# Kernel optimization log

Measured on AMD Instinct MI355X. Metric: run time of the kernel, lower is better.

## Reference

```python
import jax, jax.numpy as jnp
import numpy as np
from jax import lax

D_MODEL = 384
D_INNER = 768          # expand * d_model
D_HALF = D_INNER // 2  # 384
D_STATE = 16
D_CONV = 4
DT_RANK = 24           # ceil(384/16)
BATCH = 8
SEQLEN = 4097
EXTRAS = 1
LMAIN = SEQLEN - EXTRAS


def setup_inputs() -> dict:
    key = jax.random.key(0)
    ks = jax.random.split(key, 12)
    hidden_states = jax.random.normal(ks[0], (BATCH, SEQLEN, D_MODEL), jnp.float32)
    in_proj_w = jax.random.normal(ks[1], (D_INNER, D_MODEL), jnp.float32) * 0.02
    conv_x_w = jax.random.normal(ks[2], (D_HALF, 1, D_CONV), jnp.float32) * 0.2
    conv_z_w = jax.random.normal(ks[3], (D_HALF, 1, D_CONV), jnp.float32) * 0.2
    x_proj_w = jax.random.normal(ks[4], (DT_RANK + 2 * D_STATE, D_HALF), jnp.float32) * 0.02
    dt_std = DT_RANK ** -0.5
    dt_proj_w = jax.random.uniform(ks[5], (D_HALF, DT_RANK), jnp.float32, -dt_std, dt_std)
    # bias = inverse softplus of dt sampled log-uniform in [1e-3, 1e-1]
    dt = jnp.exp(jax.random.uniform(ks[6], (D_HALF,), jnp.float32)
                 * (jnp.log(0.1) - jnp.log(0.001)) + jnp.log(0.001))
    dt = jnp.clip(dt, 1e-4, None)
    dt_proj_b = dt + jnp.log(-jnp.expm1(-dt))
    A_log = jnp.log(jnp.broadcast_to(jnp.arange(1, D_STATE + 1, dtype=jnp.float32),
                                     (D_HALF, D_STATE)))
    D_param = jnp.ones((D_HALF,), jnp.float32)
    out_proj_w = jax.random.normal(ks[7], (D_MODEL, D_HALF), jnp.float32) * 0.02
    perm = jax.random.permutation(ks[8], LMAIN).astype(jnp.int64)
    perm_rev = jnp.argsort(perm).astype(jnp.int64)
    return {
        "hidden_states": hidden_states,
        "in_proj_w": in_proj_w,
        "conv_x_w": conv_x_w,
        "conv_z_w": conv_z_w,
        "x_proj_w": x_proj_w,
        "dt_proj_w": dt_proj_w,
        "dt_proj_b": dt_proj_b,
        "A_log": A_log,
        "D_param": D_param,
        "out_proj_w": out_proj_w,
        "perm": perm,
        "perm_rev": perm_rev,
    }


def _depthwise_conv_same(x, w):
    # x: (B, C, L), w: (C, 1, K); torch padding='same' for k=4 -> pad (left=1, right=2)
    total = D_CONV - 1
    left = total // 2
    return lax.conv_general_dilated(
        x, w, window_strides=(1,), padding=[(left, total - left)],
        dimension_numbers=("NCH", "OIH", "NCH"), feature_group_count=D_HALF)


def _selective_scan(x, dt, A, Bm, Cm, D_param, delta_bias):
    # x, dt: (B, d, L); A: (d, n); Bm, Cm: (B, n, L)
    dt = jax.nn.softplus(dt + delta_bias[None, :, None])
    xT = jnp.moveaxis(x, 2, 0)    # (L, B, d)
    dtT = jnp.moveaxis(dt, 2, 0)  # (L, B, d)
    BT = jnp.moveaxis(Bm, 2, 0)   # (L, B, n)
    CT = jnp.moveaxis(Cm, 2, 0)   # (L, B, n)

    def step(h, inp):
        x_t, dt_t, B_t, C_t = inp
        dA = jnp.exp(dt_t[..., None] * A)                      # (B, d, n)
        h = h * dA + (dt_t * x_t)[..., None] * B_t[:, None, :]  # (B, d, n)
        y = jnp.einsum("bdn,bn->bd", h, C_t)
        return h, y

    h0 = jnp.zeros((x.shape[0], x.shape[1], A.shape[1]), x.dtype)
    _, ys = lax.scan(step, h0, (xT, dtT, BT, CT))
    y = jnp.moveaxis(ys, 0, 2)  # (B, d, L)
    return y + D_param[None, :, None] * x


def reference(hidden_states, in_proj_w, conv_x_w, conv_z_w, x_proj_w,
              dt_proj_w, dt_proj_b, A_log, D_param, out_proj_w, perm, perm_rev):
    # in_proj (no bias): (B,L,D) -> (B, d_inner, L)
    xz = jnp.einsum("bld,ed->bel", hidden_states, in_proj_w)
    # hilbert/zigzag reorder on the main (non-extra) tokens
    xz = jnp.concatenate([xz[:, :, :EXTRAS], xz[:, :, EXTRAS:][:, :, perm]], axis=2)

    x, z = jnp.split(xz, 2, axis=1)  # (B, d_half, L) each
    A = -jnp.exp(A_log)
    x = jax.nn.silu(_depthwise_conv_same(x, conv_x_w))
    z = jax.nn.silu(_depthwise_conv_same(z, conv_z_w))

    x_dbl = jnp.einsum("bdl,ed->bel", x, x_proj_w)  # (B, dt_rank+2n, L)
    dt_low, Bm, Cm = jnp.split(x_dbl, [DT_RANK, DT_RANK + D_STATE], axis=1)
    dt = jnp.einsum("brl,dr->bdl", dt_low, dt_proj_w)

    y = _selective_scan(x, dt, A, Bm, Cm, D_param, dt_proj_b)
    y = (y * z).transpose(0, 2, 1)  # (B, L, d_half)
    out = jnp.einsum("bld,ed->ble", y, out_proj_w)  # (B, L, D)
    # undo the permutation on the output
    out = jnp.concatenate([out[:, :EXTRAS], out[:, EXTRAS:][:, perm_rev]], axis=1)
    return out
```

## Files before the change

### kernel.cpp

```cpp
#include <hip/hip_runtime.h>
#include <hip/hip_bf16.h>

#define DEVI __device__ __forceinline__

constexpr int B_   = 8;
constexpr int L_   = 4097;
constexpr int MTOT = B_ * L_;
constexpr int DH   = 384;
constexpr int NS   = 16;
constexpr int CH   = 48;
constexpr int NCH  = (L_ + CH - 1) / CH;

typedef __bf16 bf16x8 __attribute__((ext_vector_type(8)));
typedef float  f32x4  __attribute__((ext_vector_type(4)));

DEVI float bl(unsigned v) { return __uint_as_float(v << 16); }
DEVI float bh(unsigned v) { return __uint_as_float(v & 0xffff0000u); }
DEVI float bf(const __hip_bfloat16 x) { return __bfloat162float(x); }
DEVI unsigned short f2bu(float x) {
  __hip_bfloat16 b = __float2bfloat16(x);
  return *(unsigned short*)&b;
}
DEVI float u16f(const uint4& u, int j) {
  const unsigned w = (&u.x)[j >> 1];
  return (j & 1) ? bh(w) : bl(w);
}
DEVI float softplus_f(float x) {
  return (x > 20.f) ? x : __logf(1.f + __expf(x));
}

DEVI void gld16(const __hip_bfloat16* g, __hip_bfloat16* l) {
  __builtin_amdgcn_global_load_lds(
      (const __attribute__((address_space(1))) void*)g,
      (__attribute__((address_space(3))) void*)l, 16, 0, 0);
}

__global__ void flag_k(const void* hs, int* flagp) {
  if (threadIdx.x == 0 && blockIdx.x == 0) {
    const unsigned short* u = (const unsigned short*)hs;
    int ok = 1;
    for (int i = 0; i < 8; ++i) {
      const unsigned short v = u[2 * i];
      const int e = (v >> 7) & 0xFF;
      if (!(v == 0 || (e >= 100 && e <= 140))) ok = 0;
    }
    flagp[0] = ok;
    flagp[1] = 1;
  }
}

__global__ void a2prep_k(const void* __restrict__ alog, float* __restrict__ a2fo,
                         int* flagp) {
  const int d = threadIdx.x;
  const int f = flagp[0];
  float a2[16];
#pragma unroll
  for (int n = 0; n < 16; ++n) {
    const float v = f ? bf(((const __hip_bfloat16*)alog)[d * 16 + n])
                      : ((const float*)alog)[d * 16 + n];
    a2[n] = -1.4426950408889634f * __expf(v);
    a2fo[d * 16 + n] = a2[n];
  }
  int ok = 1;
#pragma unroll
  for (int n = 1; n < 16; ++n) {
    const float ref = (float)(n + 1) * a2[0];
    if (fabsf(a2[n] - ref) > 1e-3f * fabsf(ref)) ok = 0;
  }
  if (!ok) atomicAnd(&flagp[1], 0);
}

__global__ void perm_k(const int* p0, const int* p1, int* d0, int* d1) {
  __shared__ int s_or;
  const int* src = blockIdx.x ? p1 : p0;
  int*       dst = blockIdx.x ? d1 : d0;
  if (threadIdx.x == 0) s_or = 0;
  __syncthreads();
  int loc = 0;
  for (int i = threadIdx.x; i < 2048; i += 1024) loc |= src[2 * i + 1];
  atomicOr(&s_or, loc);
  __syncthreads();
  const bool is64 = (s_or == 0);
  for (int j = threadIdx.x; j < 4096; j += 1024)
    dst[j] = is64 ? (int)((const long long*)src)[j] : src[j];
}

struct NormSet { const void* src[8]; void* dst[8]; int n[8]; };
__global__ void norm_all(NormSet s, const int* flagp) {
  const int idx = blockIdx.x * 256 + threadIdx.x;
  const int f = flagp[0];
#pragma unroll
  for (int t = 0; t < 8; ++t) {
    if (idx < s.n[t]) {
      __hip_bfloat16* d = (__hip_bfloat16*)s.dst[t];
      if (f) d[idx] = ((const __hip_bfloat16*)s.src[t])[idx];
      else   d[idx] = __float2bfloat16(((const float*)s.src[t])[idx]);
    }
  }
}

__global__ void prep_k(const __hip_bfloat16* __restrict__ dtw,
                       const __hip_bfloat16* __restrict__ xw,
                       __hip_bfloat16* __restrict__ wcomb) {
  const int idx = blockIdx.x * 256 + threadIdx.x;
  if (idx >= 512 * 384) return;
  const int n = idx / 384, k = idx - n * 384;
  float v = 0.f;
  if (n < 384) {
#pragma unroll
    for (int r = 0; r < 24; ++r) v += bf(dtw[n * 24 + r]) * bf(xw[r * 384 + k]);
  } else if (n < 416) {
    v = bf(xw[(24 + n - 384) * 384 + k]);
  }
  wcomb[idx] = __float2bfloat16(v);
}

__global__ void cvt_k(const void* __restrict__ hs, __hip_bfloat16* __restrict__ dst,
                      const int* __restrict__ gidx, const int* __restrict__ flagp) {
  const int idx = blockIdx.x * 256 + threadIdx.x;
  if (idx >= MTOT * 48) return;
  const int j = idx % 48;
  const int r = idx / 48;
  const int b = r / L_, t = r - b * L_;
  const int src = b * L_ + (t == 0 ? 0 : 1 + gidx[t - 1]);
  uint4 o;
  if (flagp[0]) {
    o = *(const uint4*)((const __hip_bfloat16*)hs + (size_t)src * 384 + j * 8);
  } else {
    const float* f = (const float*)hs + (size_t)src * 384 + j * 8;
    const float4 f0 = *(const float4*)f;
    const float4 f1 = *(const float4*)(f + 4);
    o.x = f2bu(f0.x) | ((unsigned)f2bu(f0.y) << 16);
    o.y = f2bu(f0.z) | ((unsigned)f2bu(f0.w) << 16);
    o.z = f2bu(f1.x) | ((unsigned)f2bu(f1.y) << 16);
    o.w = f2bu(f1.z) | ((unsigned)f2bu(f1.w) << 16);
  }
  *(uint4*)(dst + (size_t)r * 384 + j * 8) = o;
}

template<int GATHER, int EPI>
__global__ __launch_bounds__(256, 3)
void gemm_k(const __hip_bfloat16* __restrict__ A, const __hip_bfloat16* __restrict__ W,
            void* __restrict__ e0, void* __restrict__ e1,
            const __hip_bfloat16* __restrict__ bias,
            const int* __restrict__ gidx, const int* __restrict__ flagp,
            int M, int N)
{
  __shared__ __align__(16) __hip_bfloat16 lA[128 * 32];
  __shared__ __align__(16) __hip_bfloat16 lB[128 * 32];
  const int tid  = threadIdx.x;
  const int lane = tid & 63;
  const int wv   = tid >> 6;
  const int wm   = wv >> 1, wn = wv & 1;
  const int lrow = lane & 15, quad = lane >> 4;
  const int fbf  = flagp[0];

  const int NT = gridDim.x;
  const int nblocks = NT * (int)gridDim.y;
  const int id = blockIdx.y * NT + blockIdx.x;
  const int q8 = nblocks >> 3, r8 = nblocks & 7;
  const int xcd = id & 7, slot = id >> 3;
  const int nid = (xcd < r8 ? xcd * (q8 + 1)
                            : r8 * (q8 + 1) + (xcd - r8) * q8) + slot;
  const int mt = nid / NT, nt = nid - mt * NT;

  const bool live = !(EPI == 1 && nt * 128 + wn * 64 >= 416);

  const __hip_bfloat16* aSrc[2];
  const __hip_bfloat16* bSrc[2];
  __hip_bfloat16* aDst[2];
  __hip_bfloat16* bDst[2];
#pragma unroll
  for (int p = 0; p < 2; ++p) {
    const int row = p * 64 + (tid >> 2);
    const int kc  = (tid & 3) * 8;
    int r = mt * 128 + row;
    if (r >= M) r = M - 1;
    int src;
    if (GATHER) { const int b = r / L_, t = r - b * L_;
                  src = b * L_ + (t == 0 ? 0 : 1 + gidx[t - 1]); }
    else        { src = r; }
    aSrc[p] = A + (size_t)src * 384 + kc;
    const int c = nt * 128 + row;
    bSrc[p] = W + (size_t)c * 384 + kc;
    aDst[p] = &lA[(p * 256 + tid) * 8];
    bDst[p] = &lB[(p * 256 + tid) * 8];
  }

  f32x4 acc[4][4] = {};

#pragma unroll
  for (int kt = 0; kt < 12; ++kt) {
    __syncthreads();
#pragma unroll
    for (int p = 0; p < 2; ++p) gld16(aSrc[p] + kt * 32, aDst[p]);
#pragma unroll
    for (int p = 0; p < 2; ++p) gld16(bSrc[p] + kt * 32, bDst[p]);
    __syncthreads();
    if (live) {
      bf16x8 af[4], bfr[4];
#pragma unroll
      for (int i = 0; i < 4; ++i)
        af[i] = *reinterpret_cast<const bf16x8*>(&lA[(wm * 64 + i * 16 + lrow) * 32 + quad * 8]);
#pragma unroll
      for (int j = 0; j < 4; ++j)
        bfr[j] = *reinterpret_cast<const bf16x8*>(&lB[(wn * 64 + j * 16 + lrow) * 32 + quad * 8]);
#pragma unroll
      for (int i = 0; i < 4; ++i)
#pragma unroll
        for (int j = 0; j < 4; ++j)
          acc[i][j] = __builtin_amdgcn_mfma_f32_16x16x32_bf16(af[i], bfr[j], acc[i][j], 0, 0, 0);
    }
  }

#pragma unroll
  for (int i = 0; i < 4; ++i) {
    const int row0 = mt * 128 + wm * 64 + i * 16 + quad * 4;
#pragma unroll
    for (int j = 0; j < 4; ++j) {
      const int col = nt * 128 + wn * 64 + j * 16 + lrow;
      if (col >= N) continue;
#pragma unroll
      for (int rg = 0; rg < 4; ++rg) {
        const int r = row0 + rg;
        if (r >= M) continue;
        const float v = acc[i][j][rg];
        if (EPI == 0) {
          if (col < 384) ((__hip_bfloat16*)e0)[(size_t)r * 384 + col] = __float2bfloat16(v);
          else           ((__hip_bfloat16*)e1)[(size_t)r * 384 + (col - 384)] = __float2bfloat16(v);
        } else if (EPI == 1) {
          if (col < 384) {
            const float sp = softplus_f(v + bf(bias[col]));
            ((__hip_bfloat16*)e0)[(size_t)r * 384 + col] = __float2bfloat16(sp);
          } else if (col < 416) {
            ((float*)e1)[(size_t)r * 32 + (col - 384)] = v;
          }
        } else {
          if (fbf) ((__hip_bfloat16*)e0)[(size_t)r * 384 + col] = __float2bfloat16(v);
          else     ((float*)e0)[(size_t)r * 384 + col] = v;
        }
      }
    }
  }
}

__global__ void convx_k(const __hip_bfloat16* __restrict__ xh,
                        const __hip_bfloat16* __restrict__ cxw,
                        __hip_bfloat16* __restrict__ xc) {
  const int idx = blockIdx.x * 256 + threadIdx.x;
  if (idx >= MTOT * 48) return;
  const int g  = idx % 48;
  const int rg = idx / 48;
  const int t  = rg % L_;
  const int c0 = g * 8;
  uint4 wv[4];
#pragma unroll
  for (int p = 0; p < 4; ++p) wv[p] = *(const uint4*)(cxw + c0 * 4 + p * 8);
  float acc[8] = {};
#pragma unroll
  for (int k = 0; k < 4; ++k) {
    const int tt = t + k - 1;
    if (tt < 0 || tt >= L_) continue;
    const uint4 u = *(const uint4*)(xh + (size_t)(rg + k - 1) * 384 + c0);
#pragma unroll
    for (int j = 0; j < 8; ++j) {
      const int e = j * 4 + k;
      acc[j] += u16f(wv[e >> 3], e & 7) * u16f(u, j);
    }
  }
  uint4 o;
#pragma unroll
  for (int p = 0; p < 4; ++p) {
    const float s0 = acc[2 * p]     / (1.f + __expf(-acc[2 * p]));
    const float s1 = acc[2 * p + 1] / (1.f + __expf(-acc[2 * p + 1]));
    (&o.x)[p] = f2bu(s0) | ((unsigned)f2bu(s1) << 16);
  }
  *(uint4*)(xc + (size_t)rg * 384 + c0) = o;
}

__global__ __launch_bounds__(128)
void scan1_k(const __hip_bfloat16* __restrict__ dt, const float* __restrict__ bc,
             __hip_bfloat16* xcio,
             const float* __restrict__ a2f,
             const __hip_bfloat16* __restrict__ dpar,
             float* __restrict__ pbuf, float* __restrict__ hend,
             const int* __restrict__ flagp)
{
  __shared__ __align__(16) float lBC[CH * 32];
  const int blk = blockIdx.x;
  const int dt3 = blk % 3;
  const int c   = (blk / 3) % NCH;
  const int b   = blk / (3 * NCH);
  const int d   = dt3 * 128 + threadIdx.x;
  const int t0  = c * CH;
  const int r0  = b * L_ + t0;
  const int tmax = (L_ - t0 < CH) ? (L_ - t0) : CH;
  for (int i = threadIdx.x; i < tmax * 32; i += 128) lBC[i] = bc[(size_t)r0 * 32 + i];
  __syncthreads();

  float h[16];
#pragma unroll
  for (int n = 0; n < 16; ++n) h[n] = 0.f;
  float sdt = 0.f;
  const float Dd = bf(dpar[d]);
  const size_t base = ((size_t)(c * 8 + b) * 16) * 384 + d;

  if (flagp[1]) {
    const float a2b = a2f[d * 16];
    for (int tt = 0; tt < tmax; ++tt) {
      const size_t r = (size_t)(r0 + tt);
      const float dtv = bf(dt[r * 384 + d]);
      const float xv  = bf(xcio[r * 384 + d]);
      sdt += dtv;
      const float dtx = dtv * xv;
      float pw[17];
      pw[1] = exp2f(dtv * a2b);
#pragma unroll
      for (int n = 2; n <= 16; ++n) pw[n] = pw[n >> 1] * pw[n - (n >> 1)];
      float4 bq[4], cq[4];
#pragma unroll
      for (int q = 0; q < 4; ++q) {
        bq[q] = *(const float4*)&lBC[tt * 32 + q * 4];
        cq[q] = *(const float4*)&lBC[tt * 32 + 16 + q * 4];
      }
      float y = 0.f;
#pragma unroll
      for (int n = 0; n < 16; ++n) {
        h[n] = h[n] * pw[n + 1] + dtx * (&bq[n >> 2].x)[n & 3];
        y += h[n] * (&cq[n >> 2].x)[n & 3];
      }
      y += Dd * xv;
      xcio[r * 384 + d] = __float2bfloat16(y);
    }
    float Ep[17];
    Ep[1] = exp2f(sdt * a2b);
#pragma unroll
    for (int n = 2; n <= 16; ++n) Ep[n] = Ep[n >> 1] * Ep[n - (n >> 1)];
#pragma unroll
    for (int n = 0; n < 16; ++n) {
      pbuf[base + n * 384] = Ep[n + 1];
      hend[base + n * 384] = h[n];
    }
  } else {
    float a2[16];
#pragma unroll
    for (int n = 0; n < 16; ++n) a2[n] = a2f[d * 16 + n];
    for (int tt = 0; tt < tmax; ++tt) {
      const size_t r = (size_t)(r0 + tt);
      const float dtv = bf(dt[r * 384 + d]);
      const float xv  = bf(xcio[r * 384 + d]);
      sdt += dtv;
      const float dtx = dtv * xv;
      float4 bq[4], cq[4];
#pragma unroll
      for (int q = 0; q < 4; ++q) {
        bq[q] = *(const float4*)&lBC[tt * 32 + q * 4];
        cq[q] = *(const float4*)&lBC[tt * 32 + 16 + q * 4];
      }
      float y = 0.f;
#pragma unroll
      for (int n = 0; n < 16; ++n) {
        h[n] = h[n] * exp2f(dtv * a2[n]) + dtx * (&bq[n >> 2].x)[n & 3];
        y += h[n] * (&cq[n >> 2].x)[n & 3];
      }
      y += Dd * xv;
      xcio[r * 384 + d] = __float2bfloat16(y);
    }
#pragma unroll
    for (int n = 0; n < 16; ++n) {
      pbuf[base + n * 384] = exp2f(sdt * a2[n]);
      hend[base + n * 384] = h[n];
    }
  }
}

__global__ void scan2_k(float* __restrict__ pbuf, const float* __restrict__ hend) {
  const int tid = blockIdx.x * 256 + threadIdx.x;
  const int d = tid % 384;
  const int n = (tid / 384) & 15;
  const int b = tid / 6144;
  float H = 0.f;
  for (int c = 0; c < NCH; ++c) {
    const size_t idx = ((size_t)(c * 8 + b) * 16 + n) * 384 + d;
    const float p = pbuf[idx];
    const float he = hend[idx];
    pbuf[idx] = H;
    H = p * H + he;
  }
}

__global__ __launch_bounds__(128)
void scan3_k(__hip_bfloat16* dtyg, const float* __restrict__ bc,
             const __hip_bfloat16* __restrict__ yl,
             const __hip_bfloat16* __restrict__ zh,
             const __hip_bfloat16* __restrict__ czw,
             const float* __restrict__ a2f,
             const float* __restrict__ hstart,
             const int* __restrict__ flagp)
{
  __shared__ __align__(16) float lC[CH * 16];
  const int blk = blockIdx.x;
  const int dt3 = blk % 3;
  const int c   = (blk / 3) % NCH;
  const int b   = blk / (3 * NCH);
  const int d   = dt3 * 128 + threadIdx.x;
  const int t0  = c * CH;
  const int r0  = b * L_ + t0;
  const int tmax = (L_ - t0 < CH) ? (L_ - t0) : CH;
  for (int i = threadIdx.x; i < tmax * 16; i += 128)
    lC[i] = bc[(size_t)r0 * 32 + (i >> 4) * 32 + 16 + (i & 15)];
  __syncthreads();

  float hs_[16];
  const size_t base = ((size_t)(c * 8 + b) * 16) * 384 + d;
#pragma unroll
  for (int n = 0; n < 16; ++n) hs_[n] = hstart[base + n * 384];
  float cw[4];
#pragma unroll
  for (int k = 0; k < 4; ++k) cw[k] = bf(czw[d * 4 + k]);

  float zm1 = (t0 - 1 >= 0) ? bf(zh[(size_t)(r0 - 1) * 384 + d]) : 0.f;
  float z0  = bf(zh[(size_t)r0 * 384 + d]);
  float zp1 = (t0 + 1 < L_) ? bf(zh[(size_t)(r0 + 1) * 384 + d]) : 0.f;
  float sdt = 0.f;

  if (flagp[1]) {
    const float a2b = a2f[d * 16];
    for (int tt = 0; tt < tmax; ++tt) {
      const int t = t0 + tt;
      const size_t r = (size_t)(r0 + tt);
      const float zp2 = (t + 2 < L_) ? bf(zh[(r + 2) * 384 + d]) : 0.f;
      const float dtv = bf(dtyg[r * 384 + d]);
      sdt += dtv;
      float pw[17];
      pw[1] = exp2f(sdt * a2b);
#pragma unroll
      for (int n = 2; n <= 16; ++n) pw[n] = pw[n >> 1] * pw[n - (n >> 1)];
      float4 cq[4];
#pragma unroll
      for (int q = 0; q < 4; ++q) cq[q] = *(const float4*)&lC[tt * 16 + q * 4];
      float corr = 0.f;
#pragma unroll
      for (int n = 0; n < 16; ++n)
        corr += (&cq[n >> 2].x)[n & 3] * hs_[n] * pw[n + 1];
      const float y = bf(yl[r * 384 + d]) + corr;
      const float zc = cw[0] * zm1 + cw[1] * z0 + cw[2] * zp1 + cw[3] * zp2;
      const float zs = zc / (1.f + __expf(-zc));
      dtyg[r * 384 + d] = __float2bfloat16(y * zs);
      zm1 = z0; z0 = zp1; zp1 = zp2;
    }
  } else {
    float a2[16];
#pragma unroll
    for (int n = 0; n < 16; ++n) a2[n] = a2f[d * 16 + n];
    for (int tt = 0; tt < tmax; ++tt) {
      const int t = t0 + tt;
      const size_t r = (size_t)(r0 + tt);
      const float zp2 = (t + 2 < L_) ? bf(zh[(r + 2) * 384 + d]) : 0.f;
      const float dtv = bf(dtyg[r * 384 + d]);
      sdt += dtv;
      float4 cq[4];
#pragma unroll
      for (int q = 0; q < 4; ++q) cq[q] = *(const float4*)&lC[tt * 16 + q * 4];
      float corr = 0.f;
#pragma unroll
      for (int n = 0; n < 16; ++n)
        corr += (&cq[n >> 2].x)[n & 3] * hs_[n] * exp2f(sdt * a2[n]);
      const float y = bf(yl[r * 384 + d]) + corr;
      const float zc = cw[0] * zm1 + cw[1] * z0 + cw[2] * zp1 + cw[3] * zp2;
      const float zs = zc / (1.f + __expf(-zc));
      dtyg[r * 384 + d] = __float2bfloat16(y * zs);
      zm1 = z0; z0 = zp1; zp1 = zp2;
    }
  }
}

extern "C" void kernel_launch(void* const* d_in, const int* in_sizes, int n_in,
                              void* d_out, int out_size, void* d_ws, size_t ws_size,
                              hipStream_t stream) {
  const void* hs   = d_in[0];
  const void* w_in = d_in[1];
  const void* cxw  = d_in[2];
  const void* czw  = d_in[3];
  const void* xw   = d_in[4];
  const void* dtw  = d_in[5];
  const void* dtb  = d_in[6];
  const void* alog = d_in[7];
  const void* dpar = d_in[8];
  const void* ow   = d_in[9];
  const int* perm  = (const int*)d_in[10];
  const int* permr = (const int*)d_in[11];

  char* ws = (char*)d_ws;
  size_t off = 0;
  auto alloc = [&](size_t nbytes) -> char* {
    char* p = ws + off;
    off += (nbytes + 255) & ~(size_t)255;
    return p;
  };
  int* flag              = (int*)alloc(256);
  int* nperm             = (int*)alloc(4096 * 4);
  int* npermr            = (int*)alloc(4096 * 4);
  float* a2f             = (float*)alloc(6144 * 4);
  __hip_bfloat16* w_inb  = (__hip_bfloat16*)alloc(294912 * 2);
  __hip_bfloat16* cxwb   = (__hip_bfloat16*)alloc(1536 * 2);
  __hip_bfloat16* czwb   = (__hip_bfloat16*)alloc(1536 * 2);
  __hip_bfloat16* xwb    = (__hip_bfloat16*)alloc(21504 * 2);
  __hip_bfloat16* dtwb   = (__hip_bfloat16*)alloc(9216 * 2);
  __hip_bfloat16* dtbb   = (__hip_bfloat16*)alloc(384 * 2);
  __hip_bfloat16* dparb  = (__hip_bfloat16*)alloc(384 * 2);
  __hip_bfloat16* owb    = (__hip_bfloat16*)alloc(147456 * 2);
  __hip_bfloat16* wcombb = (__hip_bfloat16*)alloc((size_t)512 * 384 * 2);
  __hip_bfloat16* hsb    = (__hip_bfloat16*)alloc((size_t)MTOT * 384 * 2);
  __hip_bfloat16* zh     = (__hip_bfloat16*)alloc((size_t)MTOT * 384 * 2);
  __hip_bfloat16* xc     = (__hip_bfloat16*)alloc((size_t)MTOT * 384 * 2);
  __hip_bfloat16* dtyg   = (__hip_bfloat16*)alloc((size_t)MTOT * 384 * 2);
  float*          bcf    = (float*)alloc((size_t)MTOT * 32 * 4);
  __hip_bfloat16* xh   = (__hip_bfloat16*)d_out;
  float*          pbuf = (float*)d_out;
  float*          hend = (float*)((char*)d_out + (size_t)NCH * B_ * NS * DH * 4);

  flag_k<<<1, 64, 0, stream>>>(hs, flag);
  perm_k<<<2, 1024, 0, stream>>>(perm, permr, nperm, npermr);
  a2prep_k<<<1, 384, 0, stream>>>(alog, a2f, flag);
  NormSet ns;
  ns.src[0] = w_in; ns.dst[0] = w_inb; ns.n[0] = 294912;
  ns.src[1] = ow;   ns.dst[1] = owb;   ns.n[1] = 147456;
  ns.src[2] = xw;   ns.dst[2] = xwb;   ns.n[2] = 21504;
  ns.src[3] = dtw;  ns.dst[3] = dtwb;  ns.n[3] = 9216;
  ns.src[4] = cxw;  ns.dst[4] = cxwb;  ns.n[4] = 1536;
  ns.src[5] = czw;  ns.dst[5] = czwb;  ns.n[5] = 1536;
  ns.src[6] = dtb;  ns.dst[6] = dtbb;  ns.n[6] = 384;
  ns.src[7] = dpar; ns.dst[7] = dparb; ns.n[7] = 384;
  norm_all<<<1152, 256, 0, stream>>>(ns, flag);
  prep_k<<<768, 256, 0, stream>>>(dtwb, xwb, wcombb);
  cvt_k<<<(MTOT * 48 + 255) / 256, 256, 0, stream>>>(hs, hsb, nperm, flag);
  gemm_k<0, 0><<<dim3(6, 257), 256, 0, stream>>>(
      hsb, w_inb, xh, zh, nullptr, nullptr, flag, MTOT, 768);
  convx_k<<<(MTOT * 48 + 255) / 256, 256, 0, stream>>>(xh, cxwb, xc);
  gemm_k<0, 1><<<dim3(4, 257), 256, 0, stream>>>(
      xc, wcombb, dtyg, bcf, dtbb, nullptr, flag, MTOT, 512);
  scan1_k<<<B_ * NCH * 3, 128, 0, stream>>>(dtyg, bcf, xc, a2f, dparb, pbuf, hend, flag);
  scan2_k<<<192, 256, 0, stream>>>(pbuf, hend);
  scan3_k<<<B_ * NCH * 3, 128, 0, stream>>>(dtyg, bcf, xc, zh, czwb, a2f, pbuf, flag);
  gemm_k<1, 2><<<dim3(3, 257), 256, 0, stream>>>(
      dtyg, owb, d_out, nullptr, nullptr, npermr, flag, MTOT, 384);
  (void)in_sizes; (void)n_in; (void)out_size; (void)ws_size;
}
```

Before: 384.5 us.

## Deepen GEMM K-tile, stage epilogue through LDS, split scan reductions, shrink chunk

The GEMM now loads a K-slice of 64 per iteration, halving the syncthreads-bounded steps. Its epilogue stages accumulators through shared memory so global stores become coalesced 16-byte writes instead of scattered scalar bf16/float stores, with softplus and bias applied before staging. The scan kernels split each 16-term dot-product reduction into two accumulators to shorten the dependent add chain. The scan chunk length drops from 48 to 33, giving more parallel chunks at the cost of more carry-propagation work and larger intermediate buffers. Shared memory per GEMM block grows to 36 KB, which may limit occupancy under the launch bound of 3 blocks.

```diff
diff --git a/kernel.cpp b/kernel.cpp
--- a/kernel.cpp
+++ b/kernel.cpp
@@ -8,7 +8,7 @@
 constexpr int MTOT = B_ * L_;
 constexpr int DH   = 384;
 constexpr int NS   = 16;
-constexpr int CH   = 48;
+constexpr int CH   = 33;
 constexpr int NCH  = (L_ + CH - 1) / CH;
 
 typedef __bf16 bf16x8 __attribute__((ext_vector_type(8)));
@@ -146,8 +146,9 @@
             const int* __restrict__ gidx, const int* __restrict__ flagp,
             int M, int N)
 {
-  __shared__ __align__(16) __hip_bfloat16 lA[128 * 32];
-  __shared__ __align__(16) __hip_bfloat16 lB[128 * 32];
+  __shared__ __align__(16) char smem[36864];
+  __hip_bfloat16* lA = (__hip_bfloat16*)smem;
+  __hip_bfloat16* lB = lA + 2 * 128 * 32;
   const int tid  = threadIdx.x;
   const int lane = tid & 63;
   const int wv   = tid >> 6;
@@ -166,14 +167,16 @@
 
   const bool live = !(EPI == 1 && nt * 128 + wn * 64 >= 416);
 
-  const __hip_bfloat16* aSrc[2];
-  const __hip_bfloat16* bSrc[2];
-  __hip_bfloat16* aDst[2];
-  __hip_bfloat16* bDst[2];
-#pragma unroll
-  for (int p = 0; p < 2; ++p) {
-    const int row = p * 64 + (tid >> 2);
-    const int kc  = (tid & 3) * 8;
+  const __hip_bfloat16* aSrc[4];
+  const __hip_bfloat16* bSrc[4];
+  __hip_bfloat16* aDst[4];
+  __hip_bfloat16* bDst[4];
+#pragma unroll
+  for (int p = 0; p < 4; ++p) {
+    const int s   = p * 256 + tid;
+    const int kh  = s >> 9;
+    const int row = (s >> 2) & 127;
+    const int kc  = kh * 32 + (s & 3) * 8;
     int r = mt * 128 + row;
     if (r >= M) r = M - 1;
     int src;
@@ -181,63 +184,122 @@
                   src = b * L_ + (t == 0 ? 0 : 1 + gidx[t - 1]); }
     else        { src = r; }
     aSrc[p] = A + (size_t)src * 384 + kc;
-    const int c = nt * 128 + row;
-    bSrc[p] = W + (size_t)c * 384 + kc;
-    aDst[p] = &lA[(p * 256 + tid) * 8];
-    bDst[p] = &lB[(p * 256 + tid) * 8];
+    bSrc[p] = W + (size_t)(nt * 128 + row) * 384 + kc;
+    aDst[p] = &lA[s * 8];
+    bDst[p] = &lB[s * 8];
   }
 
   f32x4 acc[4][4] = {};
 
 #pragma unroll
-  for (int kt = 0; kt < 12; ++kt) {
+  for (int kt = 0; kt < 6; ++kt) {
     __syncthreads();
 #pragma unroll
-    for (int p = 0; p < 2; ++p) gld16(aSrc[p] + kt * 32, aDst[p]);
-#pragma unroll
-    for (int p = 0; p < 2; ++p) gld16(bSrc[p] + kt * 32, bDst[p]);
+    for (int p = 0; p < 4; ++p) gld16(aSrc[p] + kt * 64, aDst[p]);
+#pragma unroll
+    for (int p = 0; p < 4; ++p) gld16(bSrc[p] + kt * 64, bDst[p]);
     __syncthreads();
     if (live) {
-      bf16x8 af[4], bfr[4];
-#pragma unroll
-      for (int i = 0; i < 4; ++i)
-        af[i] = *reinterpret_cast<const bf16x8*>(&lA[(wm * 64 + i * 16 + lrow) * 32 + quad * 8]);
-#pragma unroll
-      for (int j = 0; j < 4; ++j)
-        bfr[j] = *reinterpret_cast<const bf16x8*>(&lB[(wn * 64 + j * 16 + lrow) * 32 + quad * 8]);
-#pragma unroll
-      for (int i = 0; i < 4; ++i)
+#pragma unroll
+      for (int kh = 0; kh < 2; ++kh) {
+        bf16x8 af[4], bfr[4];
+#pragma unroll
+        for (int i = 0; i < 4; ++i)
+          af[i] = *reinterpret_cast<const bf16x8*>(
+              &lA[kh * 4096 + (wm * 64 + i * 16 + lrow) * 32 + quad * 8]);
 #pragma unroll
         for (int j = 0; j < 4; ++j)
-          acc[i][j] = __builtin_amdgcn_mfma_f32_16x16x32_bf16(af[i], bfr[j], acc[i][j], 0, 0, 0);
-    }
-  }
-
-#pragma unroll
-  for (int i = 0; i < 4; ++i) {
-    const int row0 = mt * 128 + wm * 64 + i * 16 + quad * 4;
-#pragma unroll
-    for (int j = 0; j < 4; ++j) {
-      const int col = nt * 128 + wn * 64 + j * 16 + lrow;
-      if (col >= N) continue;
-#pragma unroll
-      for (int rg = 0; rg < 4; ++rg) {
-        const int r = row0 + rg;
-        if (r >= M) continue;
-        const float v = acc[i][j][rg];
-        if (EPI == 0) {
-          if (col < 384) ((__hip_bfloat16*)e0)[(size_t)r * 384 + col] = __float2bfloat16(v);
-          else           ((__hip_bfloat16*)e1)[(size_t)r * 384 + (col - 384)] = __float2bfloat16(v);
-        } else if (EPI == 1) {
-          if (col < 384) {
-            const float sp = softplus_f(v + bf(bias[col]));
-            ((__hip_bfloat16*)e0)[(size_t)r * 384 + col] = __float2bfloat16(sp);
-          } else if (col < 416) {
-            ((float*)e1)[(size_t)r * 32 + (col - 384)] = v;
-          }
-        } else {
-          if (fbf) ((__hip_bfloat16*)e0)[(size_t)r * 384 + col] = __float2bfloat16(v);
-          else     ((float*)e0)[(size_t)r * 384 + col] = v;
+          bfr[j] = *reinterpret_cast<const bf16x8*>(
+              &lB[kh * 4096 + (wn * 64 + j * 16 + lrow) * 32 + quad * 8]);
+#pragma unroll
+        for (int i = 0; i < 4; ++i)
+#pragma unroll
+          for (int j = 0; j < 4; ++j)
+            acc[i][j] = __builtin_amdgcn_mfma_f32_16x16x32_bf16(af[i], bfr[j], acc[i][j], 0, 0, 0);
+      }
+    }
+  }
+
+  const int r0c = mt * 128;
+  if (EPI == 1 && nt == 3) {
+#pragma unroll
+    for (int i = 0; i < 4; ++i) {
+      const int row0 = r0c + wm * 64 + i * 16 + quad * 4;
+#pragma unroll
+      for (int j = 0; j < 4; ++j) {
+        const int col = 384 + wn * 64 + j * 16 + lrow;
+        if (col >= 416) continue;
+#pragma unroll
+        for (int rg = 0; rg < 4; ++rg) {
+          const int r = row0 + rg;
+          if (r >= M) continue;
+          ((float*)e1)[(size_t)r * 32 + (col - 384)] = acc[i][j][rg];
+        }
+      }
+    }
+  } else if (EPI == 2 && !fbf) {
+    float* lT = (float*)smem;
+#pragma unroll
+    for (int h = 0; h < 2; ++h) {
+      __syncthreads();
+      if (wn == h) {
+#pragma unroll
+        for (int i = 0; i < 4; ++i)
+#pragma unroll
+          for (int j = 0; j < 4; ++j)
+#pragma unroll
+            for (int rg = 0; rg < 4; ++rg)
+              lT[(wm * 64 + i * 16 + quad * 4 + rg) * 72 + j * 16 + lrow] = acc[i][j][rg];
+      }
+      __syncthreads();
+#pragma unroll
+      for (int p = 0; p < 8; ++p) {
+        const int ch = p * 256 + tid;
+        const int row = ch >> 4, c4 = (ch & 15) * 4;
+        const int r = r0c + row;
+        if (r < M) {
+          const float4 v = *(const float4*)&lT[row * 72 + c4];
+          *(float4*)((float*)e0 + (size_t)r * 384 + nt * 128 + h * 64 + c4) = v;
+        }
+      }
+    }
+  } else {
+    __hip_bfloat16* lT = (__hip_bfloat16*)smem;
+#pragma unroll
+    for (int h = 0; h < 2; ++h) {
+      __syncthreads();
+      if (wn == h) {
+        float bj[4] = {};
+        if (EPI == 1) {
+#pragma unroll
+          for (int j = 0; j < 4; ++j)
+            bj[j] = bf(bias[nt * 128 + h * 64 + j * 16 + lrow]);
+        }
+#pragma unroll
+        for (int i = 0; i < 4; ++i)
+#pragma unroll
+          for (int j = 0; j < 4; ++j)
+#pragma unroll
+            for (int rg = 0; rg < 4; ++rg) {
+              float v = acc[i][j][rg];
+              if (EPI == 1) v = softplus_f(v + bj[j]);
+              lT[(wm * 64 + i * 16 + quad * 4 + rg) * 72 + j * 16 + lrow] =
+                  __float2bfloat16(v);
+            }
+      }
+      __syncthreads();
+#pragma unroll
+      for (int p = 0; p < 4; ++p) {
+        const int ch = p * 256 + tid;
+        const int row = ch >> 3, c8 = (ch & 7) * 8;
+        const int r = r0c + row;
+        if (r < M) {
+          const uint4 v = *(const uint4*)&lT[row * 72 + c8];
+          const int g = nt * 128 + h * 64 + c8;
+          __hip_bfloat16* dst = (EPI == 0 && g >= 384)
+                ? (__hip_bfloat16*)e1 + (size_t)r * 384 + (g - 384)
+                : (__hip_bfloat16*)e0 + (size_t)r * 384 + g;
+          *(uint4*)dst = v;
         }
       }
     }
@@ -323,13 +385,14 @@
         bq[q] = *(const float4*)&lBC[tt * 32 + q * 4];
         cq[q] = *(const float4*)&lBC[tt * 32 + 16 + q * 4];
       }
-      float y = 0.f;
+      float ya = 0.f, yb = 0.f;
 #pragma unroll
       for (int n = 0; n < 16; ++n) {
         h[n] = h[n] * pw[n + 1] + dtx * (&bq[n >> 2].x)[n & 3];
-        y += h[n] * (&cq[n >> 2].x)[n & 3];
-      }
-      y += Dd * xv;
+        const float t = h[n] * (&cq[n >> 2].x)[n & 3];
+        if (n & 1) yb += t; else ya += t;
+      }
+      const float y = ya + yb + Dd * xv;
       xcio[r * 384 + d] = __float2bfloat16(y);
     }
     float Ep[17];
@@ -357,13 +420,14 @@
         bq[q] = *(const float4*)&lBC[tt * 32 + q * 4];
         cq[q] = *(const float4*)&lBC[tt * 32 + 16 + q * 4];
       }
-      float y = 0.f;
+      float ya = 0.f, yb = 0.f;
 #pragma unroll
       for (int n = 0; n < 16; ++n) {
         h[n] = h[n] * exp2f(dtv * a2[n]) + dtx * (&bq[n >> 2].x)[n & 3];
-        y += h[n] * (&cq[n >> 2].x)[n & 3];
-      }
-      y += Dd * xv;
+        const float t = h[n] * (&cq[n >> 2].x)[n & 3];
+        if (n & 1) yb += t; else ya += t;
+      }
+      const float y = ya + yb + Dd * xv;
       xcio[r * 384 + d] = __float2bfloat16(y);
     }
 #pragma unroll
@@ -439,11 +503,13 @@
       float4 cq[4];
 #pragma unroll
       for (int q = 0; q < 4; ++q) cq[q] = *(const float4*)&lC[tt * 16 + q * 4];
-      float corr = 0.f;
-#pragma unroll
-      for (int n = 0; n < 16; ++n)
-        corr += (&cq[n >> 2].x)[n & 3] * hs_[n] * pw[n + 1];
-      const float y = bf(yl[r * 384 + d]) + corr;
+      float ca = 0.f, cb = 0.f;
+#pragma unroll
+      for (int n = 0; n < 16; ++n) {
+        const float t2 = (&cq[n >> 2].x)[n & 3] * hs_[n] * pw[n + 1];
+        if (n & 1) cb += t2; else ca += t2;
+      }
+      const float y = bf(yl[r * 384 + d]) + ca + cb;
       const float zc = cw[0] * zm1 + cw[1] * z0 + cw[2] * zp1 + cw[3] * zp2;
       const float zs = zc / (1.f + __expf(-zc));
       dtyg[r * 384 + d] = __float2bfloat16(y * zs);
@@ -462,11 +528,13 @@
       float4 cq[4];
 #pragma unroll
       for (int q = 0; q < 4; ++q) cq[q] = *(const float4*)&lC[tt * 16 + q * 4];
-      float corr = 0.f;
-#pragma unroll
-      for (int n = 0; n < 16; ++n)
-        corr += (&cq[n >> 2].x)[n & 3] * hs_[n] * exp2f(sdt * a2[n]);
-      const float y = bf(yl[r * 384 + d]) + corr;
+      float ca = 0.f, cb = 0.f;
+#pragma unroll
+      for (int n = 0; n < 16; ++n) {
+        const float t2 = (&cq[n >> 2].x)[n & 3] * hs_[n] * exp2f(sdt * a2[n]);
+        if (n & 1) cb += t2; else ca += t2;
+      }
+      const float y = bf(yl[r * 384 + d]) + ca + cb;
       const float zc = cw[0] * zm1 + cw[1] * z0 + cw[2] * zp1 + cw[3] * zp2;
       const float zs = zc / (1.f + __expf(-zc));
       dtyg[r * 384 + d] = __float2bfloat16(y * zs);
```

After: 330.6 us. 1.16x faster.
